# Kernel tuning notes

Hardware: AMD Instinct MI355X
Metric: run time of the kernel (lower is better)

## Reference

```python
import jax, jax.numpy as jnp
import numpy as np

GRID_SIZE = 16
SPLINE_ORDER = 4
GRID_LO, GRID_HI = -1.0, 1.0
NUM_GRID = 2 * SPLINE_ORDER + GRID_SIZE + 1  # 25 knots
NUM_COEFFS = GRID_SIZE + SPLINE_ORDER        # 20 basis functions
B, IN_F, OUT_F = 2048, 512, 512


def _make_grid():
    h = (GRID_HI - GRID_LO) / GRID_SIZE
    t1 = -SPLINE_ORDER * h + GRID_LO
    t2 = (GRID_SIZE + SPLINE_ORDER + 1) * h + GRID_LO
    return jnp.linspace(t1, t2, NUM_GRID)


def _bspline_basis(x, grid):
    # x: [..., in]; returns [..., in, NUM_COEFFS] via De Boor recursion
    xe = x[..., None]
    bases = ((xe >= grid[:-1]) & (xe < grid[1:])).astype(x.dtype)
    for k in range(1, SPLINE_ORDER + 1):
        left = (xe - grid[:-k - 1]) / (grid[k:-1] - grid[:-k - 1]) * bases[..., :-1]
        right = (grid[k + 1:] - xe) / (grid[k + 1:] - grid[1:-k]) * bases[..., 1:]
        bases = left + right
    return bases


def setup_inputs() -> dict:
    key = jax.random.key(0)
    ks = jax.random.split(key, 5)
    fan = np.sqrt(1.0 / IN_F)
    return {
        "x": jax.random.normal(ks[0], (B, IN_F), jnp.float32),
        "prelu_weight": jax.random.normal(ks[1], (OUT_F, IN_F), jnp.float32) * 0.25,
        "base_weight": jax.random.uniform(ks[2], (OUT_F, IN_F), jnp.float32, -fan, fan),
        "spline_weight": jax.random.uniform(ks[3], (OUT_F, IN_F), jnp.float32, -fan, fan),
        "spline_coeffs": jax.random.normal(ks[4], (OUT_F, IN_F, NUM_COEFFS), jnp.float32) * 0.1,
    }


def reference(x, prelu_weight, base_weight, spline_weight, spline_coeffs):
    grid = _make_grid()
    xc = jnp.clip(x, GRID_LO, GRID_HI)
    pos = jax.nn.relu(xc)
    neg = xc - pos
    # base path: sum_j base_w[i,j]*(prelu_w[i,j]*neg[b,j] + pos[b,j])
    # fused: never materialize the [out, B, in] prelu output
    base = neg @ (base_weight * prelu_weight).T + pos @ base_weight.T  # [B, out]
    basis = _bspline_basis(xc, grid)  # [B, in, K]
    # spline path: fold spline_weight into coeffs, single contraction over (j,k)
    eff_coeffs = spline_weight[:, :, None] * spline_coeffs  # [out, in, K]
    spline = jnp.einsum('bjk,ijk->bi', basis, eff_coeffs)   # [B, out]
    return base + spline
```

## Files before the change

kernel.cpp:

```cpp
#include <hip/hip_runtime.h>


typedef _Float16 half_t;
typedef __attribute__((ext_vector_type(8))) _Float16 half8;
typedef __attribute__((ext_vector_type(4))) float floatx4;

#define B_DIM   2048
#define J_DIM   512
#define O_DIM   512
#define SLOTS   22
#define K_TOT   (J_DIM * SLOTS)
#define MTILE   128
#define NTILE   128
#define BK      32
#define KSPLIT  11
#define KS_LEN  (K_TOT / KSPLIT)
#define KCH     (KS_LEN / BK)
#define ZERO_BLKS 64

__device__ __forceinline__ void bspline5(float xc, int& k0, float Nv[5]) {
    const float invS = 7.68f;
    float u = (xc + 1.5f) * invS;
    int m = (int)u;
    m = min(max(m, 3), 19);
    k0 = m - 4;
    Nv[0] = 1.f; Nv[1] = 0.f; Nv[2] = 0.f; Nv[3] = 0.f; Nv[4] = 0.f;
#pragma unroll
    for (int d = 1; d <= 4; ++d) {
        float nw[5];
        float inv_d = 1.0f / (float)d;
#pragma unroll
        for (int r = 0; r < 5; ++r) {
            if (r > d) { nw[r] = 0.f; continue; }
            float kk = (float)(m - d + r);
            float acc = 0.f;
            if (r >= 1) acc += (u - kk) * Nv[r - 1];
            if (r < d)  acc += (kk + (float)(d + 1) - u) * Nv[r];
            nw[r] = acc * inv_d;
        }
#pragma unroll
        for (int r = 0; r < 5; ++r) Nv[r] = nw[r];
    }
}

__global__ __launch_bounds__(256) void prep_all(const float* __restrict__ x,
                                                const float* __restrict__ pw,
                                                const float* __restrict__ bw,
                                                const float* __restrict__ sw,
                                                const float* __restrict__ sc,
                                                half_t* __restrict__ A,
                                                half_t* __restrict__ Ct,
                                                float* __restrict__ out) {
    __shared__ half_t rec[J_DIM * SLOTS];
    int bid = blockIdx.x;
    int t = threadIdx.x;

    if (bid < ZERO_BLKS) {
        float4* o = (float4*)out;
        int base = bid * 4096;
#pragma unroll
        for (int i = 0; i < 16; ++i)
            o[base + i * 256 + t] = make_float4(0.f, 0.f, 0.f, 0.f);
        return;
    }

    if (bid < ZERO_BLKS + O_DIM) {
        int i = bid - ZERO_BLKS;
#pragma unroll
        for (int jj = 0; jj < 2; ++jj) {
            int j = t + jj * 256;
            size_t ij = (size_t)i * J_DIM + j;
            float s = sw[ij], b = bw[ij], p = pw[ij];
            const float4* scp4 = (const float4*)(sc + ij * 20);
            half_t* r = rec + j * SLOTS;
#pragma unroll
            for (int v = 0; v < 5; ++v) {
                float4 c4 = scp4[v];
                r[v * 4 + 0] = (half_t)(s * c4.x);
                r[v * 4 + 1] = (half_t)(s * c4.y);
                r[v * 4 + 2] = (half_t)(s * c4.z);
                r[v * 4 + 3] = (half_t)(s * c4.w);
            }
            r[20] = (half_t)(b * p);
            r[21] = (half_t)b;
        }
        __syncthreads();
        const uint4* src = (const uint4*)rec;
        uint4* dst = (uint4*)(Ct + (size_t)i * K_TOT);
        for (int idx = t; idx < (J_DIM * SLOTS * 2) / 16; idx += 256) dst[idx] = src[idx];
        return;
    }

    int b = bid - ZERO_BLKS - O_DIM;
#pragma unroll
    for (int jj = 0; jj < 2; ++jj) {
        int j = t + jj * 256;
        float xv = x[(size_t)b * J_DIM + j];
        float xc = fminf(fmaxf(xv, -1.f), 1.f);
        float pos = fmaxf(xc, 0.f);
        float neg = xc - pos;
        int k0; float Nv[5];
        bspline5(xc, k0, Nv);
        half_t* r = rec + j * SLOTS;
#pragma unroll
        for (int k = 0; k < 20; ++k) r[k] = (half_t)0.f;
#pragma unroll
        for (int rr = 0; rr < 5; ++rr) {
            int k = k0 + rr;
            if (k >= 0) r[k] = (half_t)Nv[rr];
        }
        r[20] = (half_t)neg;
        r[21] = (half_t)pos;
    }
    __syncthreads();
    const uint4* src = (const uint4*)rec;
    uint4* dst = (uint4*)(A + (size_t)b * K_TOT);
    for (int i = t; i < (J_DIM * SLOTS * 2) / 16; i += 256) dst[i] = src[i];
}

__global__ __launch_bounds__(256, 4) void gemm_f16(const half_t* __restrict__ A,
                                                   const half_t* __restrict__ Bt,
                                                   float* __restrict__ out) {
    __shared__ half_t As[2][MTILE * BK];
    __shared__ half_t Bs[2][NTILE * BK];

    int m0 = blockIdx.x * MTILE;
    int n0 = blockIdx.y * NTILE;
    int ks = blockIdx.z * KS_LEN;

    int t = threadIdx.x;
    int w = t >> 6;
    int l = t & 63;
    int wm = w >> 1, wn = w & 1;

    floatx4 acc[4][4] = {};

    int lrow = l >> 2;
    int lkof = (((l & 3) ^ ((l >> 3) & 3)) * 8);

    const half_t* gA = A + (size_t)m0 * K_TOT + ks;
    const half_t* gB = Bt + (size_t)n0 * K_TOT + ks;

    int q = l >> 4;
    int fr = l & 15;
    int qs = (q ^ ((fr >> 1) & 3)) * 8;

#define ISSUE_LOADS(c, p)                                                     \
    {                                                                         \
        int kb = (c) * BK;                                                    \
        _Pragma("unroll")                                                     \
        for (int n = 0; n < 2; ++n) {                                         \
            int r = (w * 2 + n) * 16 + lrow;                                  \
            __builtin_amdgcn_global_load_lds(                                 \
                (const __attribute__((address_space(1))) unsigned int*)       \
                    (gA + (size_t)r * K_TOT + kb + lkof),                     \
                (__attribute__((address_space(3))) unsigned int*)             \
                    (&As[p][0] + (w * 2 + n) * 512),                          \
                16, 0, 0);                                                    \
            __builtin_amdgcn_global_load_lds(                                 \
                (const __attribute__((address_space(1))) unsigned int*)       \
                    (gB + (size_t)r * K_TOT + kb + lkof),                     \
                (__attribute__((address_space(3))) unsigned int*)             \
                    (&Bs[p][0] + (w * 2 + n) * 512),                          \
                16, 0, 0);                                                    \
        }                                                                     \
    }

    ISSUE_LOADS(0, 0)
    int p = 0;
    for (int c = 0; c < KCH; ++c) {
        __syncthreads();
        if (c + 1 < KCH) ISSUE_LOADS(c + 1, p ^ 1)

        half8 af[4], bf[4];
#pragma unroll
        for (int mt = 0; mt < 4; ++mt)
            af[mt] = *(const half8*)(&As[p][0] + (wm * 64 + mt * 16 + fr) * BK + qs);
#pragma unroll
        for (int nt = 0; nt < 4; ++nt)
            bf[nt] = *(const half8*)(&Bs[p][0] + (wn * 64 + nt * 16 + fr) * BK + qs);
#pragma unroll
        for (int mt = 0; mt < 4; ++mt)
#pragma unroll
            for (int nt = 0; nt < 4; ++nt)
                acc[mt][nt] = __builtin_amdgcn_mfma_f32_16x16x32_f16(
                    af[mt], bf[nt], acc[mt][nt], 0, 0, 0);
        p ^= 1;
    }
#undef ISSUE_LOADS

#pragma unroll
    for (int mt = 0; mt < 4; ++mt)
#pragma unroll
        for (int nt = 0; nt < 4; ++nt) {
            int rr = m0 + wm * 64 + mt * 16 + q * 4;
            int cc = n0 + wn * 64 + nt * 16 + fr;
#pragma unroll
            for (int r = 0; r < 4; ++r)
                atomicAdd(out + (size_t)(rr + r) * O_DIM + cc, acc[mt][nt][r]);
        }
}

__global__ __launch_bounds__(256) void kan_fallback(const float* __restrict__ x,
                                                    const float* __restrict__ pw,
                                                    const float* __restrict__ bw,
                                                    const float* __restrict__ sw,
                                                    const float* __restrict__ sc,
                                                    float* __restrict__ out) {
    __shared__ float s_neg[J_DIM], s_pos[J_DIM], s_bas[J_DIM][5];
    __shared__ int s_k0[J_DIM];
    int b = blockIdx.x;
    int t = threadIdx.x;
#pragma unroll
    for (int jj = 0; jj < 2; ++jj) {
        int j = t + jj * 256;
        float xv = x[(size_t)b * J_DIM + j];
        float xc = fminf(fmaxf(xv, -1.f), 1.f);
        float pos = fmaxf(xc, 0.f);
        s_pos[j] = pos;
        s_neg[j] = xc - pos;
        int k0; float Nv[5];
        bspline5(xc, k0, Nv);
        s_k0[j] = k0;
#pragma unroll
        for (int r = 0; r < 5; ++r) s_bas[j][r] = Nv[r];
    }
    __syncthreads();
    for (int i = t; i < O_DIM; i += 256) {
        float acc = 0.f;
        for (int j = 0; j < J_DIM; ++j) {
            size_t ij = (size_t)i * J_DIM + j;
            float bwv = bw[ij];
            acc += bwv * (pw[ij] * s_neg[j] + s_pos[j]);
            int k0 = s_k0[j];
            const float* cp = sc + ij * 20;
            float sp = 0.f;
#pragma unroll
            for (int r = 0; r < 5; ++r) {
                int k = k0 + r;
                if (k >= 0) sp += s_bas[j][r] * cp[k];
            }
            acc += sw[ij] * sp;
        }
        out[(size_t)b * O_DIM + i] = acc;
    }
}

extern "C" void kernel_launch(void* const* d_in, const int* in_sizes, int n_in,
                              void* d_out, int out_size, void* d_ws, size_t ws_size,
                              hipStream_t stream) {
    const float* x  = (const float*)d_in[0];
    const float* pw = (const float*)d_in[1];
    const float* bw = (const float*)d_in[2];
    const float* sw = (const float*)d_in[3];
    const float* sc = (const float*)d_in[4];
    float* out = (float*)d_out;

    const size_t ws_needed = (size_t)(B_DIM + O_DIM) * K_TOT * sizeof(half_t);
    if (ws_size < ws_needed) {
        kan_fallback<<<B_DIM, 256, 0, stream>>>(x, pw, bw, sw, sc, out);
        return;
    }

    half_t* A  = (half_t*)d_ws;
    half_t* Ct = A + (size_t)B_DIM * K_TOT;

    prep_all<<<ZERO_BLKS + O_DIM + B_DIM, 256, 0, stream>>>(x, pw, bw, sw, sc, A, Ct, out);
    dim3 g(B_DIM / MTILE, O_DIM / NTILE, KSPLIT);
    gemm_f16<<<g, 256, 0, stream>>>(A, Ct, out);
}
```

Baseline: 142.8 us.

## Use single-wave 64x64 GEMM blocks with triple-buffered async LDS loads

Restructures the split-K GEMM so each block is one wavefront computing a 64x64 tile, with a three-stage LDS ring fed by direct global-to-LDS loads and synchronised by vmcnt waits instead of block barriers. The split-K factor is also reduced from 11 to 8, lowering the number of atomic partial-sum writes. The aim is to remove barrier stalls and deepen memory latency hiding, at the cost of less operand reuse per loaded tile (smaller tiles mean more global/L2 traffic).

```diff
diff --git a/kernel.cpp b/kernel.cpp
--- a/kernel.cpp
+++ b/kernel.cpp
@@ -10,10 +10,10 @@
 #define O_DIM   512
 #define SLOTS   22
 #define K_TOT   (J_DIM * SLOTS)
-#define MTILE   128
-#define NTILE   128
+#define WTILE_M 64
+#define WTILE_N 64
 #define BK      32
-#define KSPLIT  11
+#define KSPLIT  8
 #define KS_LEN  (K_TOT / KSPLIT)
 #define KCH     (KS_LEN / BK)
 #define ZERO_BLKS 64
@@ -118,23 +118,17 @@
     for (int i = t; i < (J_DIM * SLOTS * 2) / 16; i += 256) dst[i] = src[i];
 }
 
-__global__ __launch_bounds__(256, 4) void gemm_f16(const half_t* __restrict__ A,
-                                                   const half_t* __restrict__ Bt,
-                                                   float* __restrict__ out) {
-    __shared__ half_t As[2][MTILE * BK];
-    __shared__ half_t Bs[2][NTILE * BK];
-
-    int m0 = blockIdx.x * MTILE;
-    int n0 = blockIdx.y * NTILE;
+__global__ __launch_bounds__(64, 2) void gemm_f16(const half_t* __restrict__ A,
+                                                  const half_t* __restrict__ Bt,
+                                                  float* __restrict__ out) {
+    __shared__ half_t As[3][WTILE_M * BK];
+    __shared__ half_t Bs[3][WTILE_N * BK];
+
+    int m0 = blockIdx.x * WTILE_M;
+    int n0 = blockIdx.y * WTILE_N;
     int ks = blockIdx.z * KS_LEN;
 
-    int t = threadIdx.x;
-    int w = t >> 6;
-    int l = t & 63;
-    int wm = w >> 1, wn = w & 1;
-
-    floatx4 acc[4][4] = {};
-
+    int l = threadIdx.x;
     int lrow = l >> 2;
     int lkof = (((l & 3) ^ ((l >> 3) & 3)) * 8);
 
@@ -145,56 +139,78 @@
     int fr = l & 15;
     int qs = (q ^ ((fr >> 1) & 3)) * 8;
 
+    floatx4 acc[4][4] = {};
+
 #define ISSUE_LOADS(c, p)                                                     \
     {                                                                         \
         int kb = (c) * BK;                                                    \
         _Pragma("unroll")                                                     \
-        for (int n = 0; n < 2; ++n) {                                         \
-            int r = (w * 2 + n) * 16 + lrow;                                  \
+        for (int rt = 0; rt < 4; ++rt) {                                      \
+            int r = rt * 16 + lrow;                                           \
             __builtin_amdgcn_global_load_lds(                                 \
                 (const __attribute__((address_space(1))) unsigned int*)       \
                     (gA + (size_t)r * K_TOT + kb + lkof),                     \
                 (__attribute__((address_space(3))) unsigned int*)             \
-                    (&As[p][0] + (w * 2 + n) * 512),                          \
+                    (&As[p][0] + rt * 512),                                   \
                 16, 0, 0);                                                    \
+        }                                                                     \
+        _Pragma("unroll")                                                     \
+        for (int rt = 0; rt < 4; ++rt) {                                      \
+            int r = rt * 16 + lrow;                                           \
             __builtin_amdgcn_global_load_lds(                                 \
                 (const __attribute__((address_space(1))) unsigned int*)       \
                     (gB + (size_t)r * K_TOT + kb + lkof),                     \
                 (__attribute__((address_space(3))) unsigned int*)             \
-                    (&Bs[p][0] + (w * 2 + n) * 512),                          \
+                    (&Bs[p][0] + rt * 512),                                   \
                 16, 0, 0);                                                    \
         }                                                                     \
     }
 
+#define COMPUTE_CHUNK(p)                                                      \
+    {                                                                         \
+        half8 af[4], bf[4];                                                   \
+        _Pragma("unroll")                                                     \
+        for (int mt = 0; mt < 4; ++mt)                                        \
+            af[mt] = *(const half8*)(&As[p][0] + (mt * 16 + fr) * BK + qs);   \
+        _Pragma("unroll")                                                     \
+        for (int nt = 0; nt < 4; ++nt)                                        \
+            bf[nt] = *(const half8*)(&Bs[p][0] + (nt * 16 + fr) * BK + qs);   \
+        _Pragma("unroll")                                                     \
+        for (int mt = 0; mt < 4; ++mt)                                        \
+            _Pragma("unroll")                                                 \
+            for (int nt = 0; nt < 4; ++nt)                                    \
+                acc[mt][nt] = __builtin_amdgcn_mfma_f32_16x16x32_f16(         \
+                    af[mt], bf[nt], acc[mt][nt], 0, 0, 0);                    \
+    }
+
     ISSUE_LOADS(0, 0)
+    ISSUE_LOADS(1, 1)
+    ISSUE_LOADS(2, 2)
+
     int p = 0;
-    for (int c = 0; c < KCH; ++c) {
-        __syncthreads();
-        if (c + 1 < KCH) ISSUE_LOADS(c + 1, p ^ 1)
-
-        half8 af[4], bf[4];
-#pragma unroll
-        for (int mt = 0; mt < 4; ++mt)
-            af[mt] = *(const half8*)(&As[p][0] + (wm * 64 + mt * 16 + fr) * BK + qs);
-#pragma unroll
-        for (int nt = 0; nt < 4; ++nt)
-            bf[nt] = *(const half8*)(&Bs[p][0] + (wn * 64 + nt * 16 + fr) * BK + qs);
-#pragma unroll
-        for (int mt = 0; mt < 4; ++mt)
-#pragma unroll
-            for (int nt = 0; nt < 4; ++nt)
-                acc[mt][nt] = __builtin_amdgcn_mfma_f32_16x16x32_f16(
-                    af[mt], bf[nt], acc[mt][nt], 0, 0, 0);
-        p ^= 1;
-    }
+#pragma unroll 1
+    for (int c = 0; c < KCH - 3; ++c) {
+        asm volatile("s_waitcnt vmcnt(16)" ::: "memory");
+        COMPUTE_CHUNK(p)
+        ISSUE_LOADS(c + 3, p)
+        p = (p == 2) ? 0 : p + 1;
+    }
+    asm volatile("s_waitcnt vmcnt(16)" ::: "memory");
+    COMPUTE_CHUNK(2)
+    asm volatile("s_waitcnt vmcnt(8)" ::: "memory");
+    COMPUTE_CHUNK(0)
+    asm volatile("s_waitcnt vmcnt(0)" ::: "memory");
+    COMPUTE_CHUNK(1)
+
 #undef ISSUE_LOADS
+#undef COMPUTE_CHUNK
 
 #pragma unroll
     for (int mt = 0; mt < 4; ++mt)
 #pragma unroll
         for (int nt = 0; nt < 4; ++nt) {
-            int rr = m0 + wm * 64 + mt * 16 + q * 4;
-            int cc = n0 + wn * 64 + nt * 16 + fr;
+            int rr = m0 + mt * 16 + q * 4;
+            int cc = n0 + nt * 16 + fr;
 #pragma unroll
             for (int r = 0; r < 4; ++r)
                 atomicAdd(out + (size_t)(rr + r) * O_DIM + cc, acc[mt][nt][r]);
@@ -266,6 +282,6 @@
     half_t* Ct = A + (size_t)B_DIM * K_TOT;
 
     prep_all<<<ZERO_BLKS + O_DIM + B_DIM, 256, 0, stream>>>(x, pw, bw, sw, sc, A, Ct, out);
-    dim3 g(B_DIM / MTILE, O_DIM / NTILE, KSPLIT);
-    gemm_f16<<<g, 256, 0, stream>>>(A, Ct, out);
-}
+    dim3 g(B_DIM / WTILE_M, O_DIM / WTILE_N, KSPLIT);
+    gemm_f16<<<g, 64, 0, stream>>>(A, Ct, out);
+}
```

Result: slower. 156.6 us (+9.7%).
